# Performance work log

Hardware: AMD Instinct MI355X
Metric: run time of the kernel (lower is better)

## Reference

```python
import jax, jax.numpy as jnp
import numpy as np

B, T, F = 32, 4096, 64
ALPHA = 0.9


def setup_inputs() -> dict:
    key = jax.random.key(0)
    k1, = jax.random.split(key, 1)
    spectrogram = jax.random.normal(k1, (B, T, F), dtype=jnp.float32)
    # _create_frequency_tuning: logspace(log10(1000), log10(80000), n_bands) / max
    freqs = jnp.logspace(np.log10(1000.0), np.log10(80000.0), F, dtype=jnp.float32)
    frequency_tuning = freqs / freqs.max()
    compression_threshold = jnp.float32(0.1)
    compression_ratio = jnp.float32(0.5)
    return {
        "spectrogram": spectrogram,
        "frequency_tuning": frequency_tuning,
        "compression_threshold": compression_threshold,
        "compression_ratio": compression_ratio,
    }


def reference(spectrogram, frequency_tuning, compression_threshold, compression_ratio):
    # [B, T, F] * [1, 1, F]
    tuned = spectrogram * frequency_tuning[None, None, :]
    mask = (tuned > compression_threshold).astype(tuned.dtype)
    compressed = tuned * (1.0 - mask) + (
        compression_threshold + (tuned - compression_threshold) * compression_ratio
    ) * mask
    # Leaky-integrator EMA over time: y_0 = x_0; y_t = a*y_{t-1} + (1-a)*x_t
    first = compressed[:, 0, :]                      # [B, F]
    xs = jnp.moveaxis(compressed[:, 1:, :], 1, 0)    # [T-1, B, F]

    def step(carry, x):
        y = ALPHA * carry + (1.0 - ALPHA) * x
        return y, y

    _, rest = jax.lax.scan(step, first, xs)          # [T-1, B, F]
    integrated = jnp.concatenate([first[:, None, :], jnp.moveaxis(rest, 0, 1)], axis=1)
    return jax.nn.relu(integrated)
```

## Files before the change

### kernel.cpp

```cpp
#include <hip/hip_runtime.h>


typedef float vf2 __attribute__((ext_vector_type(2)));

namespace {
constexpr int kB    = 32;
constexpr int kT    = 4096;
constexpr int kF2   = 32;
constexpr int kFH   = 16;
constexpr int kL    = 16;
constexpr int kSEG  = 16;
constexpr int kTBLK = kSEG * kL;
constexpr int kGRP  = 2 * kTBLK;
constexpr int kNG   = kT / kGRP;
constexpr int kLW   = 4;
constexpr int kWROWS = kSEG * kLW;
constexpr float kA   = 0.9f;
constexpr float kOmA = 1.0f - kA;

constexpr float apow(int n) { float r = 1.f; for (int i = 0; i < n; ++i) r *= 0.9f; return r; }
constexpr float kA16 = apow(kL);
constexpr float kA4  = apow(kLW);
}

__global__ __launch_bounds__(256, 2) void cochlea_kernel(
    const vf2* __restrict__ spec,
    const vf2* __restrict__ ftune,
    const float* __restrict__ thr_p,
    const float* __restrict__ ratio_p,
    vf2* __restrict__ out)
{
    const int tid = threadIdx.x;
    const int f2  = tid & (kFH - 1);
    const int seg = tid >> 4;

    const int d    = blockIdx.x;
    const int blo  = d & 7;
    const int rest = d >> 3;
    const int b    = ((rest >> 4) << 3) | blo;
    const int sub  = rest & 15;
    const int g    = sub >> 1;
    const int fh   = sub & 1;

    const float thr   = thr_p[0];
    const float ratio = ratio_p[0];
    const vf2 ft = ftune[fh * kFH + f2];

    const size_t rowbase = (size_t)b * kT * kF2 + fh * kFH + f2;
    const int tg0 = g * kGRP;

    auto comp = [&](vf2 x) -> vf2 {
        float ta = x.x * ft.x, tc = x.y * ft.y;
        float ca = fmaf(ta - thr, ratio, thr);
        float cc = fmaf(tc - thr, ratio, thr);
        vf2 v;
        v.x = (ta > thr) ? ca : ta;
        v.y = (tc > thr) ? cc : tc;
        return v;
    };

    const vf2* sp0 = spec + rowbase + (size_t)(tg0 + seg * kL) * kF2;
    const vf2* sp1 = sp0 + (size_t)kTBLK * kF2;

    vf2 wx[kLW];
    if (g > 0) {
        const vf2* wp = spec + rowbase + (size_t)(tg0 - kWROWS + seg * kLW) * kF2;
        #pragma unroll
        for (int j = 0; j < kLW; ++j) wx[j] = wp[(size_t)j * kF2];
    }
    vf2 xv0[kL];
    #pragma unroll
    for (int j = 0; j < kL; ++j) xv0[j] = sp0[(size_t)j * kF2];
    vf2 xv1[kL];
    #pragma unroll
    for (int j = 0; j < kL; ++j) xv1[j] = sp1[(size_t)j * kF2];

    vf2 yw = {0.f, 0.f};
    if (g > 0) {
        #pragma unroll
        for (int j = 0; j < kLW; ++j) {
            vf2 v = comp(wx[j]);
            yw.x = fmaf(kA, yw.x, kOmA * v.x);
            yw.y = fmaf(kA, yw.y, kOmA * v.y);
        }
    }

    vf2 r[kL];
    vf2 y  = {0.f, 0.f};
    vf2 v0 = {0.f, 0.f};
    #pragma unroll
    for (int j = 0; j < kL; ++j) {
        vf2 v = comp(xv0[j]);
        if (j == 0) v0 = v;
        y.x = fmaf(kA, y.x, kOmA * v.x);
        y.y = fmaf(kA, y.y, kOmA * v.y);
        r[j] = y;
    }

    __shared__ vf2 lds_c[2][kSEG][kFH];
    __shared__ vf2 lds_w[kSEG][kFH];
    __shared__ vf2 lds_v0[kFH];
    lds_c[0][seg][f2] = y;
    lds_w[seg][f2] = yw;
    if (seg == 0) lds_v0[f2] = v0;
    __syncthreads();

    vf2 Hw;
    if (g == 0) {
        Hw = lds_v0[f2];
    } else {
        Hw = {0.f, 0.f};
        #pragma unroll
        for (int j = 0; j < kSEG; ++j) {
            vf2 w = lds_w[j][f2];
            Hw.x = fmaf(kA4, Hw.x, w.x);
            Hw.y = fmaf(kA4, Hw.y, w.y);
        }
    }

    vf2 acc = Hw, yin0 = {0.f, 0.f};
    #pragma unroll
    for (int j = 0; j < kSEG; ++j) {
        if (j == seg) yin0 = acc;
        vf2 c = lds_c[0][j][f2];
        acc.x = fmaf(kA16, acc.x, c.x);
        acc.y = fmaf(kA16, acc.y, c.y);
    }
    const vf2 I1 = acc;

    vf2* op0 = out + rowbase + (size_t)(tg0 + seg * kL) * kF2;
    float ap = kA;
    #pragma unroll
    for (int j = 0; j < kL; ++j) {
        vf2 o;
        o.x = fmaxf(fmaf(ap, yin0.x, r[j].x), 0.f);
        o.y = fmaxf(fmaf(ap, yin0.y, r[j].y), 0.f);
        __builtin_nontemporal_store(o, op0 + (size_t)j * kF2);
        ap *= kA;
    }

    y = {0.f, 0.f};
    #pragma unroll
    for (int j = 0; j < kL; ++j) {
        vf2 v = comp(xv1[j]);
        y.x = fmaf(kA, y.x, kOmA * v.x);
        y.y = fmaf(kA, y.y, kOmA * v.y);
        r[j] = y;
    }
    lds_c[1][seg][f2] = y;
    __syncthreads();

    vf2 acc1 = I1, yin1 = {0.f, 0.f};
    #pragma unroll
    for (int j = 0; j < kSEG; ++j) {
        if (j == seg) yin1 = acc1;
        vf2 c = lds_c[1][j][f2];
        acc1.x = fmaf(kA16, acc1.x, c.x);
        acc1.y = fmaf(kA16, acc1.y, c.y);
    }

    vf2* op1 = op0 + (size_t)kTBLK * kF2;
    ap = kA;
    #pragma unroll
    for (int j = 0; j < kL; ++j) {
        vf2 o;
        o.x = fmaxf(fmaf(ap, yin1.x, r[j].x), 0.f);
        o.y = fmaxf(fmaf(ap, yin1.y, r[j].y), 0.f);
        __builtin_nontemporal_store(o, op1 + (size_t)j * kF2);
        ap *= kA;
    }
}

extern "C" void kernel_launch(void* const* d_in, const int* in_sizes, int n_in,
                              void* d_out, int out_size, void* d_ws, size_t ws_size,
                              hipStream_t stream) {
    const vf2*   spec  = (const vf2*)d_in[0];
    const vf2*   ftune = (const vf2*)d_in[1];
    const float* thr   = (const float*)d_in[2];
    const float* ratio = (const float*)d_in[3];
    vf2* out = (vf2*)d_out;

    dim3 grid(kB * kNG * 2), block(kSEG * kFH);
    cochlea_kernel<<<grid, block, 0, stream>>>(spec, ftune, thr, ratio, out);
}
```

Measured before the change: 13.60 us.

## Walk four smaller tiles per block with double-buffered register prefetch

Each block now covers four tiles of 8 rows per thread, down from two tiles of 16. Register buffers alternate between tiles, and the loads for tile k+2 are issued while tile k is still being scanned and stored. The group size and block count stay the same. The aim is to cut register pressure and overlap global loads with compute, at the cost of more barriers and cross-segment scan passes per block.

```diff
diff --git a/kernel.cpp b/kernel.cpp
--- a/kernel.cpp
+++ b/kernel.cpp
@@ -4,23 +4,24 @@
 typedef float vf2 __attribute__((ext_vector_type(2)));
 
 namespace {
-constexpr int kB    = 32;
-constexpr int kT    = 4096;
-constexpr int kF2   = 32;
-constexpr int kFH   = 16;
-constexpr int kL    = 16;
-constexpr int kSEG  = 16;
-constexpr int kTBLK = kSEG * kL;
-constexpr int kGRP  = 2 * kTBLK;
-constexpr int kNG   = kT / kGRP;
-constexpr int kLW   = 4;
+constexpr int kB     = 32;
+constexpr int kT     = 4096;
+constexpr int kF2    = 32;
+constexpr int kFH    = 16;
+constexpr int kL     = 8;
+constexpr int kSEG   = 16;
+constexpr int kTILE  = kSEG * kL;
+constexpr int kWALK  = 4;
+constexpr int kGRP   = kWALK * kTILE;
+constexpr int kNG    = kT / kGRP;
+constexpr int kLW    = 4;
 constexpr int kWROWS = kSEG * kLW;
 constexpr float kA   = 0.9f;
 constexpr float kOmA = 1.0f - kA;
 
 constexpr float apow(int n) { float r = 1.f; for (int i = 0; i < n; ++i) r *= 0.9f; return r; }
-constexpr float kA16 = apow(kL);
-constexpr float kA4  = apow(kLW);
+constexpr float kA8 = apow(kL);
+constexpr float kA4 = apow(kLW);
 }
 
 __global__ __launch_bounds__(256, 2) void cochlea_kernel(
@@ -48,6 +49,7 @@
 
     const size_t rowbase = (size_t)b * kT * kF2 + fh * kFH + f2;
     const int tg0 = g * kGRP;
+    const vf2* spBase = spec + rowbase;
 
     auto comp = [&](vf2 x) -> vf2 {
         float ta = x.x * ft.x, tc = x.y * ft.y;
@@ -59,21 +61,21 @@
         return v;
     };
 
-    const vf2* sp0 = spec + rowbase + (size_t)(tg0 + seg * kL) * kF2;
-    const vf2* sp1 = sp0 + (size_t)kTBLK * kF2;
-
     vf2 wx[kLW];
     if (g > 0) {
-        const vf2* wp = spec + rowbase + (size_t)(tg0 - kWROWS + seg * kLW) * kF2;
+        const vf2* wp = spBase + (size_t)(tg0 - kWROWS + seg * kLW) * kF2;
         #pragma unroll
         for (int j = 0; j < kLW; ++j) wx[j] = wp[(size_t)j * kF2];
     }
-    vf2 xv0[kL];
-    #pragma unroll
-    for (int j = 0; j < kL; ++j) xv0[j] = sp0[(size_t)j * kF2];
-    vf2 xv1[kL];
-    #pragma unroll
-    for (int j = 0; j < kL; ++j) xv1[j] = sp1[(size_t)j * kF2];
+    vf2 xvA[kL], xvB[kL];
+    {
+        const vf2* sp0 = spBase + (size_t)(tg0 + 0 * kTILE + seg * kL) * kF2;
+        #pragma unroll
+        for (int j = 0; j < kL; ++j) xvA[j] = sp0[(size_t)j * kF2];
+        const vf2* sp1 = spBase + (size_t)(tg0 + 1 * kTILE + seg * kL) * kF2;
+        #pragma unroll
+        for (int j = 0; j < kL; ++j) xvB[j] = sp1[(size_t)j * kF2];
+    }
 
     vf2 yw = {0.f, 0.f};
     if (g > 0) {
@@ -85,89 +87,70 @@
         }
     }
 
-    vf2 r[kL];
-    vf2 y  = {0.f, 0.f};
-    vf2 v0 = {0.f, 0.f};
-    #pragma unroll
-    for (int j = 0; j < kL; ++j) {
-        vf2 v = comp(xv0[j]);
-        if (j == 0) v0 = v;
-        y.x = fmaf(kA, y.x, kOmA * v.x);
-        y.y = fmaf(kA, y.y, kOmA * v.y);
-        r[j] = y;
-    }
-
-    __shared__ vf2 lds_c[2][kSEG][kFH];
+    __shared__ vf2 lds_c[kWALK][kSEG][kFH];
     __shared__ vf2 lds_w[kSEG][kFH];
     __shared__ vf2 lds_v0[kFH];
-    lds_c[0][seg][f2] = y;
     lds_w[seg][f2] = yw;
-    if (seg == 0) lds_v0[f2] = v0;
-    __syncthreads();
 
-    vf2 Hw;
-    if (g == 0) {
-        Hw = lds_v0[f2];
-    } else {
-        Hw = {0.f, 0.f};
+    vf2 I = {0.f, 0.f};
+    vf2 r[kL];
+
+    #pragma unroll
+    for (int k = 0; k < kWALK; ++k) {
+        vf2* xv = (k & 1) ? xvB : xvA;
+
+        vf2 y = {0.f, 0.f};
+        #pragma unroll
+        for (int j = 0; j < kL; ++j) {
+            vf2 v = comp(xv[j]);
+            if (k == 0 && j == 0 && seg == 0) lds_v0[f2] = v;
+            y.x = fmaf(kA, y.x, kOmA * v.x);
+            y.y = fmaf(kA, y.y, kOmA * v.y);
+            r[j] = y;
+        }
+        lds_c[k][seg][f2] = y;
+        __syncthreads();
+
+        if (k == 0) {
+            if (g == 0) {
+                I = lds_v0[f2];
+            } else {
+                I = {0.f, 0.f};
+                #pragma unroll
+                for (int j = 0; j < kSEG; ++j) {
+                    vf2 w = lds_w[j][f2];
+                    I.x = fmaf(kA4, I.x, w.x);
+                    I.y = fmaf(kA4, I.y, w.y);
+                }
+            }
+        }
+
+        vf2 acc = I, yin = {0.f, 0.f};
         #pragma unroll
         for (int j = 0; j < kSEG; ++j) {
-            vf2 w = lds_w[j][f2];
-            Hw.x = fmaf(kA4, Hw.x, w.x);
-            Hw.y = fmaf(kA4, Hw.y, w.y);
+            if (j == seg) yin = acc;
+            vf2 c = lds_c[k][j][f2];
+            acc.x = fmaf(kA8, acc.x, c.x);
+            acc.y = fmaf(kA8, acc.y, c.y);
         }
-    }
+        I = acc;
 
-    vf2 acc = Hw, yin0 = {0.f, 0.f};
-    #pragma unroll
-    for (int j = 0; j < kSEG; ++j) {
-        if (j == seg) yin0 = acc;
-        vf2 c = lds_c[0][j][f2];
-        acc.x = fmaf(kA16, acc.x, c.x);
-        acc.y = fmaf(kA16, acc.y, c.y);
-    }
-    const vf2 I1 = acc;
+        if (k + 2 < kWALK) {
+            const vf2* spn = spBase + (size_t)(tg0 + (k + 2) * kTILE + seg * kL) * kF2;
+            #pragma unroll
+            for (int j = 0; j < kL; ++j) xv[j] = spn[(size_t)j * kF2];
+        }
 
-    vf2* op0 = out + rowbase + (size_t)(tg0 + seg * kL) * kF2;
-    float ap = kA;
-    #pragma unroll
-    for (int j = 0; j < kL; ++j) {
-        vf2 o;
-        o.x = fmaxf(fmaf(ap, yin0.x, r[j].x), 0.f);
-        o.y = fmaxf(fmaf(ap, yin0.y, r[j].y), 0.f);
-        __builtin_nontemporal_store(o, op0 + (size_t)j * kF2);
-        ap *= kA;
-    }
-
-    y = {0.f, 0.f};
-    #pragma unroll
-    for (int j = 0; j < kL; ++j) {
-        vf2 v = comp(xv1[j]);
-        y.x = fmaf(kA, y.x, kOmA * v.x);
-        y.y = fmaf(kA, y.y, kOmA * v.y);
-        r[j] = y;
-    }
-    lds_c[1][seg][f2] = y;
-    __syncthreads();
-
-    vf2 acc1 = I1, yin1 = {0.f, 0.f};
-    #pragma unroll
-    for (int j = 0; j < kSEG; ++j) {
-        if (j == seg) yin1 = acc1;
-        vf2 c = lds_c[1][j][f2];
-        acc1.x = fmaf(kA16, acc1.x, c.x);
-        acc1.y = fmaf(kA16, acc1.y, c.y);
-    }
-
-    vf2* op1 = op0 + (size_t)kTBLK * kF2;
-    ap = kA;
-    #pragma unroll
-    for (int j = 0; j < kL; ++j) {
-        vf2 o;
-        o.x = fmaxf(fmaf(ap, yin1.x, r[j].x), 0.f);
-        o.y = fmaxf(fmaf(ap, yin1.y, r[j].y), 0.f);
-        __builtin_nontemporal_store(o, op1 + (size_t)j * kF2);
-        ap *= kA;
+        vf2* op = out + rowbase + (size_t)(tg0 + k * kTILE + seg * kL) * kF2;
+        float ap = kA;
+        #pragma unroll
+        for (int j = 0; j < kL; ++j) {
+            vf2 o;
+            o.x = fmaxf(fmaf(ap, yin.x, r[j].x), 0.f);
+            o.y = fmaxf(fmaf(ap, yin.y, r[j].y), 0.f);
+            __builtin_nontemporal_store(o, op + (size_t)j * kF2);
+            ap *= kA;
+        }
     }
 }
 
```

Result: slower. 14.00 us (+3.0%).
